# Performance work log

Measured on AMD Instinct MI355X. Metric: run time of the kernel, lower is better.

Reference implementation:

```python
import jax, jax.numpy as jnp
import numpy as np

NEG_INF = -1e9


def setup_inputs() -> dict:
    B, S, D = 4, 2048, 1024
    key = jax.random.key(0)
    ks = jax.random.split(key, 10)
    sc = 1.0 / np.sqrt(D)
    return {
        "batch": jax.random.normal(ks[0], (B, S, D), jnp.float32),
        "padding_mask": jax.random.randint(ks[1], (B, S), 0, 2) > 0,
        "Wq": jax.random.normal(ks[2], (D, D), jnp.float32) * sc,
        "bq": jnp.zeros((D,), jnp.float32),
        "Wk": jax.random.normal(ks[3], (D, D), jnp.float32) * sc,
        "bk": jnp.zeros((D,), jnp.float32),
        "Wv": jax.random.normal(ks[4], (D, D), jnp.float32) * sc,
        "bv": jnp.zeros((D,), jnp.float32),
        "Wo": jax.random.normal(ks[5], (D, D), jnp.float32) * sc,
        "bo": jnp.zeros((D,), jnp.float32),
        "num_heads": 16,
    }


def _split_heads(x, H):
    B, S, D = x.shape
    return x.reshape(B, S, H, D // H).transpose(0, 2, 1, 3)  # [B,H,S,hd]


def reference(batch, padding_mask, Wq, bq, Wk, bk, Wv, bv, Wo, bo, num_heads):
    B, S, D = batch.shape
    H = num_heads
    q = _split_heads(batch @ Wq + bq, H)  # [B,H,S,hd]
    k = _split_heads(batch @ Wk + bk, H)
    v = _split_heads(batch @ Wv + bv, H)
    # tf.keras.layers.Attention default: unscaled dot-product scores
    scores = jnp.einsum("bhqd,bhkd->bhqk", q, k)
    kmask = padding_mask[:, None, None, :]  # value/key mask -> masks score columns
    scores = jnp.where(kmask, scores, NEG_INF)
    probs = jax.nn.softmax(scores, axis=-1)
    ctx = jnp.einsum("bhqk,bhkd->bhqd", probs, v)
    # query mask zeroes padded query positions (tf Attention behavior)
    ctx = ctx * padding_mask[:, None, :, None].astype(ctx.dtype)
    ctx = ctx.transpose(0, 2, 1, 3).reshape(B, S, D)
    return ctx @ Wo + bo
```

## Files before the change

kernel.cpp:

```cpp
#include <hip/hip_runtime.h>


#define Bb 4
#define Ss 2048
#define Dd 1024
#define Hh 16
#define SZt 8388608

typedef short bf16x8 __attribute__((ext_vector_type(8)));
typedef _Float16 f16x8 __attribute__((ext_vector_type(8)));
typedef float f32x4 __attribute__((ext_vector_type(4)));
typedef float f32x16 __attribute__((ext_vector_type(16)));
typedef unsigned int u32x4 __attribute__((ext_vector_type(4)));
typedef unsigned short u16;

__device__ __forceinline__ float bf2f(u16 u) {
    return __builtin_bit_cast(float, ((unsigned)u) << 16);
}
__device__ __forceinline__ u16 f2bf(float f) {
    unsigned u = __builtin_bit_cast(unsigned, f);
    unsigned r = 0x7FFFu + ((u >> 16) & 1u);
    return (u16)((u + r) >> 16);
}
__device__ __forceinline__ u16 f2h(float f) {
    _Float16 h = (_Float16)f;
    return __builtin_bit_cast(u16, h);
}
__device__ __forceinline__ bf16x8 ldfrag(const u16* p) {
    return __builtin_bit_cast(bf16x8, *(const uint4*)p);
}
__device__ __forceinline__ f16x8 ldfragh(const u16* p) {
    return __builtin_bit_cast(f16x8, *(const uint4*)p);
}
__device__ __forceinline__ f32x4 mfma16h(f16x8 a, f16x8 b, f32x4 c) {
    return __builtin_amdgcn_mfma_f32_16x16x32_f16(a, b, c, 0, 0, 0);
}
__device__ __forceinline__ f32x4 mfma16b(bf16x8 a, bf16x8 b, f32x4 c) {
    return __builtin_amdgcn_mfma_f32_16x16x32_bf16(a, b, c, 0, 0, 0);
}
__device__ __forceinline__ f32x16 mfma32(bf16x8 a, bf16x8 b, f32x16 c) {
    return __builtin_amdgcn_mfma_f32_32x32x16_bf16(a, b, c, 0, 0, 0);
}
__device__ __forceinline__ f32x16 mfma32h(f16x8 a, f16x8 b, f32x16 c) {
    return __builtin_amdgcn_mfma_f32_32x32x16_f16(a, b, c, 0, 0, 0);
}
__device__ __forceinline__ unsigned cvt_pk_bf16(float a, float b) {
    unsigned r;
    asm("v_cvt_pk_bf16_f32 %0, %1, %2" : "=v"(r) : "v"(a), "v"(b));
    return r;
}
__device__ __forceinline__ void gl2lds16(const u16* g, u16* l) {
    __builtin_amdgcn_global_load_lds(
        (const __attribute__((address_space(1))) u16*)g,
        (__attribute__((address_space(3))) u16*)l, 16, 0, 0);
}

__global__ void normalize_mask(const unsigned char* __restrict__ raw, float* __restrict__ out,
                               float* __restrict__ cnt, int n) {
    __shared__ int flags;
    __shared__ float scnt[Bb];
    if (threadIdx.x == 0) flags = 0;
    if (threadIdx.x < Bb) scnt[threadIdx.x] = 0.f;
    __syncthreads();
    int f = 0;
    for (int i = threadIdx.x; i < n; i += blockDim.x) {
        unsigned char c = raw[i];
        if ((i & 3) != 0 && c) f |= 1;
        if ((i & 3) == 1 && c >= 2) f |= 2;
        if ((i & 3) == 3 && c >= 2) f |= 4;
    }
    if (f) atomicOr(&flags, f);
    __syncthreads();
    int fl = flags;
    int layout;
    if (!(fl & 1)) layout = 0;
    else if (fl & 2) layout = 2;
    else if (fl & 4) layout = 3;
    else layout = 1;
    for (int i = threadIdx.x; i < n; i += blockDim.x) {
        int v;
        if (layout == 0)      v = ((const int*)raw)[i];
        else if (layout == 1) v = raw[i];
        else if (layout == 2) v = ((const u16*)raw)[i] != 0;
        else                  v = ((const unsigned*)raw)[i] != 0;
        out[i] = (v != 0) ? 1.0f : 0.0f;
        if (v == 0) atomicAdd(&scnt[i >> 11], 1.0f);
    }
    __syncthreads();
    if (threadIdx.x < Bb) cnt[threadIdx.x] = scnt[threadIdx.x];
}

__global__ void concat_bias(const float* __restrict__ a, const float* __restrict__ b,
                            const float* __restrict__ c, float* __restrict__ o) {
    int i = blockIdx.x * 256 + threadIdx.x;
    o[i] = (i < 1024) ? a[i] : ((i < 2048) ? b[i - 1024] : c[i - 2048]);
}

__global__ __launch_bounds__(256) void convert_xh(const float* __restrict__ X,
                                                  u16* __restrict__ Xh) {
    size_t i = ((size_t)blockIdx.x * 256 + threadIdx.x) * 4;
    float4 v = *(const float4*)(X + i);
    u16 h0 = f2h(v.x), h1 = f2h(v.y), h2 = f2h(v.z), h3 = f2h(v.w);
    uint2 ph = { (unsigned)h0 | ((unsigned)h1 << 16), (unsigned)h2 | ((unsigned)h3 << 16) };
    *(uint2*)(Xh + i) = ph;
}

__global__ __launch_bounds__(256) void transpose_wh(const float* __restrict__ W, u16* __restrict__ Wt) {
    __shared__ float t[32][33];
    const int tx = threadIdx.x, ty = threadIdx.y;
    const int n0 = blockIdx.x * 32, k0 = blockIdx.y * 32;
    #pragma unroll
    for (int i = 0; i < 4; i++)
        t[ty + i * 8][tx] = W[(size_t)(k0 + ty + i * 8) * Dd + n0 + tx];
    __syncthreads();
    #pragma unroll
    for (int i = 0; i < 4; i++)
        Wt[(size_t)(n0 + ty + i * 8) * Dd + k0 + tx] = f2h(t[tx][ty + i * 8]);
}
__global__ __launch_bounds__(256) void transpose_w(const float* __restrict__ W, u16* __restrict__ Wt) {
    __shared__ float t[32][33];
    const int tx = threadIdx.x, ty = threadIdx.y;
    const int n0 = blockIdx.x * 32, k0 = blockIdx.y * 32;
    #pragma unroll
    for (int i = 0; i < 4; i++)
        t[ty + i * 8][tx] = W[(size_t)(k0 + ty + i * 8) * Dd + n0 + tx];
    __syncthreads();
    #pragma unroll
    for (int i = 0; i < 4; i++)
        Wt[(size_t)(n0 + ty + i * 8) * Dd + k0 + tx] = f2bf(t[tx][ty + i * 8]);
}

__global__ __launch_bounds__(512, 2) void gemm_qkv(
    const u16* __restrict__ Ah, const u16* __restrict__ Wcat, const float* __restrict__ bcat,
    const float* __restrict__ mnorm,
    u16* __restrict__ Qb, u16* __restrict__ Kb, u16* __restrict__ Vt)
{
    __shared__ u16 As[3][256][64];
    __shared__ u16 Bs[2][128][64];
    const int tid = threadIdx.x, lane = tid & 63, wave = tid >> 6;
    const int wm = wave >> 1, wn = wave & 1;
    const int bm = blockIdx.y * 256, bn = blockIdx.x * 128;
    const bool isQ = (bn < 1024);
    const int l15 = lane & 15, lq = lane >> 4;
    const int rl = lane >> 3;
    const int s8 = ((lane & 7) ^ rl) * 8;
    const u16* agp = Ah + (size_t)(bm + wave * 32 + rl) * Dd + s8;
    const u16* bgp = Wcat + (size_t)(bn + wave * 16 + rl) * Dd + s8;

    f32x4 acc[4][4] = {};

    auto stageA = [&](int slot, int kt) {
        u16* d = &As[slot][wave * 32][0];
        const u16* g = agp + kt * 64;
        #pragma unroll
        for (int j = 0; j < 4; ++j)
            gl2lds16(g + (size_t)(j * 8) * Dd, d + j * 8 * 64);
    };
    auto stageB = [&](int slot, int kt) {
        u16* d = &Bs[slot][wave * 16][0];
        const u16* g = bgp + kt * 64;
        #pragma unroll
        for (int j = 0; j < 2; ++j)
            gl2lds16(g + (size_t)(j * 8) * Dd, d + j * 8 * 64);
    };

    stageA(0, 0); stageB(0, 0); stageA(1, 1);
    asm volatile("s_waitcnt vmcnt(4)" ::: "memory");
    __builtin_amdgcn_s_barrier();

    int cs = 0;
    for (int t = 0; t < 16; ++t) {
        if (t < 15) stageB((t + 1) & 1, t + 1);
        if (t < 14) { int ss = (cs >= 1) ? cs - 1 : cs + 2; stageA(ss, t + 2); }
        #pragma unroll
        for (int kf = 0; kf < 2; kf++) {
            f16x8 b[4], a[4];
            #pragma unroll
            for (int nt = 0; nt < 4; nt++)
                b[nt] = ldfragh(&Bs[t & 1][wn * 64 + nt * 16 + l15][(kf * 32 + lq * 8) ^ ((l15 & 7) * 8)]);
            #pragma unroll
            for (int mt = 0; mt < 4; mt++)
                a[mt] = ldfragh(&As[cs][wm * 64 + mt * 16 + l15][(kf * 32 + lq * 8) ^ ((l15 & 7) * 8)]);
            #pragma unroll
            for (int mt = 0; mt < 4; mt++)
                #pragma unroll
                for (int nt = 0; nt < 4; nt++)
                    acc[mt][nt] = mfma16h(a[mt], b[nt], acc[mt][nt]);
        }
        if (t < 14)       asm volatile("s_waitcnt vmcnt(4)" ::: "memory");
        else if (t == 14) asm volatile("s_waitcnt vmcnt(0)" ::: "memory");
        if (t < 15) __builtin_amdgcn_s_barrier();
        cs = (cs >= 2) ? 0 : cs + 1;
    }

    const float LOG2E = 1.44269504088896f;
    float bv[4];
    #pragma unroll
    for (int nt = 0; nt < 4; nt++) bv[nt] = bcat[bn + wn * 64 + nt * 16 + l15];
    #pragma unroll
    for (int mt = 0; mt < 4; mt++) {
        int r0 = bm + wm * 64 + mt * 16 + lq * 4;
        float mk[4];
        if (!isQ) {
            #pragma unroll
            for (int rr = 0; rr < 4; rr++) mk[rr] = mnorm[r0 + rr];
        }
        #pragma unroll
        for (int nt = 0; nt < 4; nt++) {
            int col = bn + wn * 64 + nt * 16 + l15;
            if (col < 1024) {
                #pragma unroll
                for (int rr = 0; rr < 4; rr++)
                    Qb[(size_t)(r0 + rr) * Dd + col] = f2h((acc[mt][nt][rr] + bv[nt]) * LOG2E);
            } else if (col < 2048) {
                int c2 = col - 1024;
                #pragma unroll
                for (int rr = 0; rr < 4; rr++)
                    Kb[(size_t)(r0 + rr) * Dd + c2] = f2h((acc[mt][nt][rr] + bv[nt]) * mk[rr]);
            } else {
                int c2 = col - 2048;
                int hh = c2 >> 6, dd = c2 & 63, b_ = r0 >> 11, s0 = r0 & 2047;
                u16 e0 = f2bf((acc[mt][nt][0] + bv[nt]) * mk[0]);
                u16 e1 = f2bf((acc[mt][nt][1] + bv[nt]) * mk[1]);
                u16 e2 = f2bf((acc[mt][nt][2] + bv[nt]) * mk[2]);
                u16 e3 = f2bf((acc[mt][nt][3] + bv[nt]) * mk[3]);
                uint2 pk = { (unsigned)e0 | ((unsigned)e1 << 16), (unsigned)e2 | ((unsigned)e3 << 16) };
                *(uint2*)(Vt + (size_t)((b_ * Hh + hh) * 64 + dd) * Ss + s0) = pk;
            }
        }
    }
}

__global__ __launch_bounds__(512, 2) void gemm_out(
    const u16* __restrict__ Ah, const u16* __restrict__ Wt,
    const float* __restrict__ bias, float* __restrict__ Cout)
{
    __shared__ u16 As[3][256][64];
    __shared__ u16 Bs[2][128][64];
    const int tid = threadIdx.x, lane = tid & 63, wave = tid >> 6;
    const int wm = wave >> 1, wn = wave & 1;
    const int bm = blockIdx.y * 256, bn = blockIdx.x * 128;
    const int l15 = lane & 15, lq = lane >> 4;
    const int rl = lane >> 3;
    const int s8 = ((lane & 7) ^ rl) * 8;
    const u16* agp = Ah + (size_t)(bm + wave * 32 + rl) * Dd + s8;
    const u16* bgp = Wt + (size_t)(bn + wave * 16 + rl) * Dd + s8;

    f32x4 acc[4][4] = {};

    auto stageA = [&](int slot, int kt) {
        u16* d = &As[slot][wave * 32][0];
        const u16* g = agp + kt * 64;
        #pragma unroll
        for (int j = 0; j < 4; ++j)
            gl2lds16(g + (size_t)(j * 8) * Dd, d + j * 8 * 64);
    };
    auto stageB = [&](int slot, int kt) {
        u16* d = &Bs[slot][wave * 16][0];
        const u16* g = bgp + kt * 64;
        #pragma unroll
        for (int j = 0; j < 2; ++j)
            gl2lds16(g + (size_t)(j * 8) * Dd, d + j * 8 * 64);
    };

    stageA(0, 0); stageB(0, 0); stageA(1, 1);
    asm volatile("s_waitcnt vmcnt(4)" ::: "memory");
    __builtin_amdgcn_s_barrier();

    int cs = 0;
    for (int t = 0; t < 16; ++t) {
        if (t < 15) stageB((t + 1) & 1, t + 1);
        if (t < 14) { int ss = (cs >= 1) ? cs - 1 : cs + 2; stageA(ss, t + 2); }
        #pragma unroll
        for (int kf = 0; kf < 2; kf++) {
            bf16x8 b[4], a[4];
            #pragma unroll
            for (int nt = 0; nt < 4; nt++)
                b[nt] = ldfrag(&Bs[t & 1][wn * 64 + nt * 16 + l15][(kf * 32 + lq * 8) ^ ((l15 & 7) * 8)]);
            #pragma unroll
            for (int mt = 0; mt < 4; mt++)
                a[mt] = ldfrag(&As[cs][wm * 64 + mt * 16 + l15][(kf * 32 + lq * 8) ^ ((l15 & 7) * 8)]);
            #pragma unroll
            for (int mt = 0; mt < 4; mt++)
                #pragma unroll
                for (int nt = 0; nt < 4; nt++)
                    acc[mt][nt] = mfma16b(a[mt], b[nt], acc[mt][nt]);
        }
        if (t < 14)       asm volatile("s_waitcnt vmcnt(4)" ::: "memory");
        else if (t == 14) asm volatile("s_waitcnt vmcnt(0)" ::: "memory");
        if (t < 15) __builtin_amdgcn_s_barrier();
        cs = (cs >= 2) ? 0 : cs + 1;
    }

    float bv[4];
    #pragma unroll
    for (int nt = 0; nt < 4; nt++) bv[nt] = bias[bn + wn * 64 + nt * 16 + l15];
    #pragma unroll
    for (int mt = 0; mt < 4; mt++) {
        int r0 = bm + wm * 64 + mt * 16 + lq * 4;
        #pragma unroll
        for (int nt = 0; nt < 4; nt++) {
            int col = bn + wn * 64 + nt * 16 + l15;
            #pragma unroll
            for (int rr = 0; rr < 4; rr++)
                Cout[(size_t)(r0 + rr) * Dd + col] = acc[mt][nt][rr] + bv[nt];
        }
    }
}

__global__ __launch_bounds__(512, 4) void attn_mfma(
    u16* qctx, const u16* __restrict__ Kb, const u16* __restrict__ Vt,
    const float* __restrict__ maskf, const float* __restrict__ cntp)
{
    __shared__ u16 Ks[64][72];
    __shared__ u16 Vs[64][72];
    __shared__ float li_s[8][32];
    const int tid = threadIdx.x, lane = tid & 63, wave = tid >> 6;
    const int l31 = lane & 31, hi = lane >> 5;
    const int bh = blockIdx.x, h = bh & 15, b = bh >> 4;
    const int q0 = blockIdx.y * 256;

    f16x8 qa[4];
    {
        const u16* qp = qctx + (size_t)(b * Ss + q0 + wave * 32 + l31) * Dd + h * 64 + hi * 8;
        #pragma unroll
        for (int kf = 0; kf < 4; kf++) qa[kf] = ldfragh(qp + kf * 16);
    }

    const int srow = tid >> 3, scol = (tid & 7) * 8;
    const u16* kgsrc = Kb + (size_t)(b * Ss + srow) * Dd + h * 64 + scol;
    const u16* vgsrc = Vt + (size_t)((b * Hh + h) * 64 + srow) * Ss + scol;
    u16* kdst = &Ks[srow][scol];
    u16* vdst = &Vs[srow][scol];

    f32x16 acc0 = {}, acc1 = {};
    float li = 0.f;

    uint4 kreg = *(const uint4*)kgsrc;
    uint4 vreg = *(const uint4*)vgsrc;

    for (int k0 = 0; k0 < Ss; k0 += 64) {
        __syncthreads();
        *(uint4*)kdst = kreg;
        *(uint4*)vdst = vreg;
        __syncthreads();
        int k0n = (k0 + 64 < Ss) ? k0 + 64 : 0;
        kreg = *(const uint4*)(kgsrc + (size_t)k0n * Dd);
        vreg = *(const uint4*)(vgsrc + k0n);

        #pragma unroll
        for (int nt = 0; nt < 2; nt++) {
            f32x16 sc = {};
            #pragma unroll
            for (int kf = 0; kf < 4; kf++) {
                f16x8 kb = ldfragh(&Ks[nt * 32 + l31][kf * 16 + hi * 8]);
                sc = mfma32h(kb, qa[kf], sc);
            }
            float p[16];
            #pragma unroll
            for (int r = 0; r < 8; r++) p[r] = __builtin_amdgcn_exp2f(sc[r]);
            li += ((p[0] + p[1]) + (p[2] + p[3])) + ((p[4] + p[5]) + (p[6] + p[7]));
            {
                unsigned w0 = cvt_pk_bf16(p[0], p[1]), w1 = cvt_pk_bf16(p[2], p[3]);
                unsigned w2 = cvt_pk_bf16(p[4], p[5]), w3 = cvt_pk_bf16(p[6], p[7]);
                auto s02 = __builtin_amdgcn_permlane32_swap((int)w0, (int)w2, false, false);
                auto s13 = __builtin_amdgcn_permlane32_swap((int)w1, (int)w3, false, false);
                u32x4 pw = { (unsigned)s02[0], (unsigned)s13[0], (unsigned)s02[1], (unsigned)s13[1] };
                bf16x8 pa0 = __builtin_bit_cast(bf16x8, pw);
                bf16x8 v00 = ldfrag(&Vs[l31][nt * 32 + hi * 8]);
                bf16x8 v10 = ldfrag(&Vs[32 + l31][nt * 32 + hi * 8]);
                acc0 = mfma32(pa0, v00, acc0);
                acc1 = mfma32(pa0, v10, acc1);
            }
            #pragma unroll
            for (int r = 8; r < 16; r++) p[r] = __builtin_amdgcn_exp2f(sc[r]);
            li += ((p[8] + p[9]) + (p[10] + p[11])) + ((p[12] + p[13]) + (p[14] + p[15]));
            {
                unsigned w4 = cvt_pk_bf16(p[8], p[9]),  w5 = cvt_pk_bf16(p[10], p[11]);
                unsigned w6 = cvt_pk_bf16(p[12], p[13]), w7 = cvt_pk_bf16(p[14], p[15]);
                auto s46 = __builtin_amdgcn_permlane32_swap((int)w4, (int)w6, false, false);
                auto s57 = __builtin_amdgcn_permlane32_swap((int)w5, (int)w7, false, false);
                u32x4 pw = { (unsigned)s46[0], (unsigned)s57[0], (unsigned)s46[1], (unsigned)s57[1] };
                bf16x8 pa1 = __builtin_bit_cast(bf16x8, pw);
                bf16x8 v01 = ldfrag(&Vs[l31][nt * 32 + 16 + hi * 8]);
                bf16x8 v11 = ldfrag(&Vs[32 + l31][nt * 32 + 16 + hi * 8]);
                acc0 = mfma32(pa1, v01, acc0);
                acc1 = mfma32(pa1, v11, acc1);
            }
        }
    }

    float li_tot = li + __shfl_xor(li, 32);
    if (hi == 0) li_s[wave][l31] = li_tot;
    __builtin_amdgcn_s_barrier();
    float cntb = cntp[b];
    #pragma unroll
    for (int g = 0; g < 4; g++) {
        float4 lv = *(const float4*)&li_s[wave][g * 8 + hi * 4];
        #pragma unroll
        for (int j = 0; j < 4; j++) {
            int r = g * 4 + j;
            int row = j + 8 * g + 4 * hi;
            int q = q0 + wave * 32 + row;
            float qm = maskf[b * Ss + q];
            float den = lv[j] - cntb;
            float rl = den > 0.f ? qm / den : 0.f;
            u16* op = qctx + (size_t)(b * Ss + q) * Dd + h * 64 + l31;
            op[0]  = f2bf(acc0[r] * rl);
            op[32] = f2bf(acc1[r] * rl);
        }
    }
}

extern "C" void kernel_launch(void* const* d_in, const int* in_sizes, int n_in,
                              void* d_out, int out_size, void* d_ws, size_t ws_size,
                              hipStream_t stream) {
    const float* X  = (const float*)d_in[0];
    const unsigned char* mr = (const unsigned char*)d_in[1];
    const float* Wq = (const float*)d_in[2];
    const float* bq = (const float*)d_in[3];
    const float* Wk = (const float*)d_in[4];
    const float* bk = (const float*)d_in[5];
    const float* Wv = (const float*)d_in[6];
    const float* bv = (const float*)d_in[7];
    const float* Wo = (const float*)d_in[8];
    const float* bo = (const float*)d_in[9];
    float* out = (float*)d_out;

    u16* wsb = (u16*)d_ws;
    u16* Xh  = wsb;
    u16* Qb  = wsb + (size_t)SZt;
    u16* Kb  = wsb + 2 * (size_t)SZt;
    u16* Vt  = wsb + 3 * (size_t)SZt;
    u16* Wot = Xh;
    u16* ob  = (u16*)d_out;
    u16* Wcat = ob + (size_t)SZt;
    u16* Wqt = Wcat;
    u16* Wkt = Wqt + 1048576;
    u16* Wvt = Wkt + 1048576;
    float* mnorm = (float*)(Wvt + 1048576);
    float* bcat  = mnorm + Bb * Ss;
    float* cntp  = bcat + 3072;

    dim3 tg(32, 32), tb(32, 8);

    normalize_mask<<<1, 1024, 0, stream>>>(mr, mnorm, cntp, Bb * Ss);
    concat_bias<<<12, 256, 0, stream>>>(bq, bk, bv, bcat);
    convert_xh<<<SZt / 1024, 256, 0, stream>>>(X, Xh);
    transpose_wh<<<tg, tb, 0, stream>>>(Wq, Wqt);
    transpose_wh<<<tg, tb, 0, stream>>>(Wk, Wkt);
    transpose_wh<<<tg, tb, 0, stream>>>(Wv, Wvt);
    gemm_qkv<<<dim3(24, 32), 512, 0, stream>>>(Xh, Wcat, bcat, mnorm, Qb, Kb, Vt);
    transpose_w<<<tg, tb, 0, stream>>>(Wo, Wot);
    attn_mfma<<<dim3(Bb * Hh, Ss / 256), 512, 0, stream>>>(Qb, Kb, Vt, mnorm, cntp);
    gemm_out<<<dim3(8, 32), 512, 0, stream>>>(Qb, Wot, bo, out);
}
```

Before: 293.8 us.

## Fuse prologue kernels, add MFMA priority hints, and widen attention key tiles

Merges the mask normalization, bias concat, X conversion and three weight transposes into one launch, cutting five kernel launches and their gaps. Wraps the MFMA sections of both GEMMs and the attention kernel in s_setprio so waves doing matrix work are issued ahead of others. The attention loop now stages 128 keys per iteration instead of 64, halving barriers per key but doubling LDS use, which may lower occupancy. The single mask block inside the large grid could become a tail if it is scheduled late.

```diff
diff --git a/kernel.cpp b/kernel.cpp
--- a/kernel.cpp
+++ b/kernel.cpp
@@ -55,68 +55,76 @@
         (__attribute__((address_space(3))) u16*)l, 16, 0, 0);
 }
 
-__global__ void normalize_mask(const unsigned char* __restrict__ raw, float* __restrict__ out,
-                               float* __restrict__ cnt, int n) {
+__global__ __launch_bounds__(256) void prologue(
+    const float* __restrict__ X, u16* __restrict__ Xh,
+    const float* __restrict__ Wq, const float* __restrict__ Wk, const float* __restrict__ Wv,
+    u16* __restrict__ Wqt, u16* __restrict__ Wkt, u16* __restrict__ Wvt,
+    const float* __restrict__ bq, const float* __restrict__ bk, const float* __restrict__ bv,
+    float* __restrict__ bcat,
+    const unsigned char* __restrict__ mraw, float* __restrict__ mnorm, float* __restrict__ cntp)
+{
+    __shared__ float tl[32][33];
     __shared__ int flags;
     __shared__ float scnt[Bb];
-    if (threadIdx.x == 0) flags = 0;
-    if (threadIdx.x < Bb) scnt[threadIdx.x] = 0.f;
-    __syncthreads();
-    int f = 0;
-    for (int i = threadIdx.x; i < n; i += blockDim.x) {
-        unsigned char c = raw[i];
-        if ((i & 3) != 0 && c) f |= 1;
-        if ((i & 3) == 1 && c >= 2) f |= 2;
-        if ((i & 3) == 3 && c >= 2) f |= 4;
-    }
-    if (f) atomicOr(&flags, f);
-    __syncthreads();
-    int fl = flags;
-    int layout;
-    if (!(fl & 1)) layout = 0;
-    else if (fl & 2) layout = 2;
-    else if (fl & 4) layout = 3;
-    else layout = 1;
-    for (int i = threadIdx.x; i < n; i += blockDim.x) {
-        int v;
-        if (layout == 0)      v = ((const int*)raw)[i];
-        else if (layout == 1) v = raw[i];
-        else if (layout == 2) v = ((const u16*)raw)[i] != 0;
-        else                  v = ((const unsigned*)raw)[i] != 0;
-        out[i] = (v != 0) ? 1.0f : 0.0f;
-        if (v == 0) atomicAdd(&scnt[i >> 11], 1.0f);
-    }
-    __syncthreads();
-    if (threadIdx.x < Bb) cnt[threadIdx.x] = scnt[threadIdx.x];
-}
-
-__global__ void concat_bias(const float* __restrict__ a, const float* __restrict__ b,
-                            const float* __restrict__ c, float* __restrict__ o) {
-    int i = blockIdx.x * 256 + threadIdx.x;
-    o[i] = (i < 1024) ? a[i] : ((i < 2048) ? b[i - 1024] : c[i - 2048]);
-}
-
-__global__ __launch_bounds__(256) void convert_xh(const float* __restrict__ X,
-                                                  u16* __restrict__ Xh) {
-    size_t i = ((size_t)blockIdx.x * 256 + threadIdx.x) * 4;
-    float4 v = *(const float4*)(X + i);
-    u16 h0 = f2h(v.x), h1 = f2h(v.y), h2 = f2h(v.z), h3 = f2h(v.w);
-    uint2 ph = { (unsigned)h0 | ((unsigned)h1 << 16), (unsigned)h2 | ((unsigned)h3 << 16) };
-    *(uint2*)(Xh + i) = ph;
-}
-
-__global__ __launch_bounds__(256) void transpose_wh(const float* __restrict__ W, u16* __restrict__ Wt) {
-    __shared__ float t[32][33];
-    const int tx = threadIdx.x, ty = threadIdx.y;
-    const int n0 = blockIdx.x * 32, k0 = blockIdx.y * 32;
-    #pragma unroll
-    for (int i = 0; i < 4; i++)
-        t[ty + i * 8][tx] = W[(size_t)(k0 + ty + i * 8) * Dd + n0 + tx];
-    __syncthreads();
-    #pragma unroll
-    for (int i = 0; i < 4; i++)
-        Wt[(size_t)(n0 + ty + i * 8) * Dd + k0 + tx] = f2h(t[tx][ty + i * 8]);
-}
+    const int blk = blockIdx.x, tid = threadIdx.x;
+
+    if (blk < 8192) {
+        size_t i = ((size_t)blk * 256 + tid) * 4;
+        float4 v = *(const float4*)(X + i);
+        u16 h0 = f2h(v.x), h1 = f2h(v.y), h2 = f2h(v.z), h3 = f2h(v.w);
+        uint2 ph = { (unsigned)h0 | ((unsigned)h1 << 16), (unsigned)h2 | ((unsigned)h3 << 16) };
+        *(uint2*)(Xh + i) = ph;
+    } else if (blk < 11264) {
+        int idx = blk - 8192;
+        int w = idx >> 10, t = idx & 1023;
+        const float* W = (w == 0) ? Wq : ((w == 1) ? Wk : Wv);
+        u16* Wt = (w == 0) ? Wqt : ((w == 1) ? Wkt : Wvt);
+        const int tx = tid & 31, ty = tid >> 5;
+        const int n0 = (t & 31) * 32, k0 = (t >> 5) * 32;
+        #pragma unroll
+        for (int i = 0; i < 4; i++)
+            tl[ty + i * 8][tx] = W[(size_t)(k0 + ty + i * 8) * Dd + n0 + tx];
+        __syncthreads();
+        #pragma unroll
+        for (int i = 0; i < 4; i++)
+            Wt[(size_t)(n0 + ty + i * 8) * Dd + k0 + tx] = f2h(tl[tx][ty + i * 8]);
+    } else if (blk < 11276) {
+        int i = (blk - 11264) * 256 + tid;
+        bcat[i] = (i < 1024) ? bq[i] : ((i < 2048) ? bk[i - 1024] : bv[i - 2048]);
+    } else {
+        const int n = Bb * Ss;
+        if (tid == 0) flags = 0;
+        if (tid < Bb) scnt[tid] = 0.f;
+        __syncthreads();
+        int f = 0;
+        for (int i = tid; i < n; i += 256) {
+            unsigned char c = mraw[i];
+            if ((i & 3) != 0 && c) f |= 1;
+            if ((i & 3) == 1 && c >= 2) f |= 2;
+            if ((i & 3) == 3 && c >= 2) f |= 4;
+        }
+        if (f) atomicOr(&flags, f);
+        __syncthreads();
+        int fl = flags;
+        int layout;
+        if (!(fl & 1)) layout = 0;
+        else if (fl & 2) layout = 2;
+        else if (fl & 4) layout = 3;
+        else layout = 1;
+        for (int i = tid; i < n; i += 256) {
+            int v;
+            if (layout == 0)      v = ((const int*)mraw)[i];
+            else if (layout == 1) v = mraw[i];
+            else if (layout == 2) v = ((const u16*)mraw)[i] != 0;
+            else                  v = ((const unsigned*)mraw)[i] != 0;
+            mnorm[i] = (v != 0) ? 1.0f : 0.0f;
+            if (v == 0) atomicAdd(&scnt[i >> 11], 1.0f);
+        }
+        __syncthreads();
+        if (tid < Bb) cntp[tid] = scnt[tid];
+    }
+}
+
 __global__ __launch_bounds__(256) void transpose_w(const float* __restrict__ W, u16* __restrict__ Wt) {
     __shared__ float t[32][33];
     const int tx = threadIdx.x, ty = threadIdx.y;
@@ -172,6 +180,7 @@
     for (int t = 0; t < 16; ++t) {
         if (t < 15) stageB((t + 1) & 1, t + 1);
         if (t < 14) { int ss = (cs >= 1) ? cs - 1 : cs + 2; stageA(ss, t + 2); }
+        __builtin_amdgcn_s_setprio(1);
         #pragma unroll
         for (int kf = 0; kf < 2; kf++) {
             f16x8 b[4], a[4];
@@ -187,6 +196,7 @@
                 for (int nt = 0; nt < 4; nt++)
                     acc[mt][nt] = mfma16h(a[mt], b[nt], acc[mt][nt]);
         }
+        __builtin_amdgcn_s_setprio(0);
         if (t < 14)       asm volatile("s_waitcnt vmcnt(4)" ::: "memory");
         else if (t == 14) asm volatile("s_waitcnt vmcnt(0)" ::: "memory");
         if (t < 15) __builtin_amdgcn_s_barrier();
@@ -271,6 +281,7 @@
     for (int t = 0; t < 16; ++t) {
         if (t < 15) stageB((t + 1) & 1, t + 1);
         if (t < 14) { int ss = (cs >= 1) ? cs - 1 : cs + 2; stageA(ss, t + 2); }
+        __builtin_amdgcn_s_setprio(1);
         #pragma unroll
         for (int kf = 0; kf < 2; kf++) {
             bf16x8 b[4], a[4];
@@ -286,6 +297,7 @@
                 for (int nt = 0; nt < 4; nt++)
                     acc[mt][nt] = mfma16b(a[mt], b[nt], acc[mt][nt]);
         }
+        __builtin_amdgcn_s_setprio(0);
         if (t < 14)       asm volatile("s_waitcnt vmcnt(4)" ::: "memory");
         else if (t == 14) asm volatile("s_waitcnt vmcnt(0)" ::: "memory");
         if (t < 15) __builtin_amdgcn_s_barrier();
@@ -312,8 +324,8 @@
     u16* qctx, const u16* __restrict__ Kb, const u16* __restrict__ Vt,
     const float* __restrict__ maskf, const float* __restrict__ cntp)
 {
-    __shared__ u16 Ks[64][72];
-    __shared__ u16 Vs[64][72];
+    __shared__ u16 Ks[128][72];
+    __shared__ u16 Vs[64][136];
     __shared__ float li_s[8][32];
     const int tid = threadIdx.x, lane = tid & 63, wave = tid >> 6;
     const int l31 = lane & 31, hi = lane >> 5;
@@ -327,35 +339,42 @@
         for (int kf = 0; kf < 4; kf++) qa[kf] = ldfragh(qp + kf * 16);
     }
 
-    const int srow = tid >> 3, scol = (tid & 7) * 8;
-    const u16* kgsrc = Kb + (size_t)(b * Ss + srow) * Dd + h * 64 + scol;
-    const u16* vgsrc = Vt + (size_t)((b * Hh + h) * 64 + srow) * Ss + scol;
-    u16* kdst = &Ks[srow][scol];
-    u16* vdst = &Vs[srow][scol];
+    const int kr = tid >> 3, kc = (tid & 7) * 8;
+    const int vd = tid >> 4, vc = (tid & 15) * 8;
+    const u16* kgb = Kb + ((size_t)b * Ss + kr) * Dd + h * 64 + kc;
+    const u16* vgb = Vt + (((size_t)(b * Hh + h)) * 64 + vd) * Ss + vc;
 
     f32x16 acc0 = {}, acc1 = {};
     float li = 0.f;
 
-    uint4 kreg = *(const uint4*)kgsrc;
-    uint4 vreg = *(const uint4*)vgsrc;
-
-    for (int k0 = 0; k0 < Ss; k0 += 64) {
-        __syncthreads();
-        *(uint4*)kdst = kreg;
-        *(uint4*)vdst = vreg;
-        __syncthreads();
-        int k0n = (k0 + 64 < Ss) ? k0 + 64 : 0;
-        kreg = *(const uint4*)(kgsrc + (size_t)k0n * Dd);
-        vreg = *(const uint4*)(vgsrc + k0n);
-
-        #pragma unroll
-        for (int nt = 0; nt < 2; nt++) {
+    uint4 kreg0 = *(const uint4*)(kgb);
+    uint4 kreg1 = *(const uint4*)(kgb + (size_t)64 * Dd);
+    uint4 vreg0 = *(const uint4*)(vgb);
+    uint4 vreg1 = *(const uint4*)(vgb + (size_t)32 * Ss);
+
+    for (int k0 = 0; k0 < Ss; k0 += 128) {
+        __syncthreads();
+        *(uint4*)&Ks[kr][kc]      = kreg0;
+        *(uint4*)&Ks[kr + 64][kc] = kreg1;
+        *(uint4*)&Vs[vd][vc]      = vreg0;
+        *(uint4*)&Vs[vd + 32][vc] = vreg1;
+        __syncthreads();
+        int k0n = (k0 + 128 < Ss) ? k0 + 128 : 0;
+        kreg0 = *(const uint4*)(kgb + (size_t)k0n * Dd);
+        kreg1 = *(const uint4*)(kgb + (size_t)(k0n + 64) * Dd);
+        vreg0 = *(const uint4*)(vgb + k0n);
+        vreg1 = *(const uint4*)(vgb + (size_t)32 * Ss + k0n);
+
+        #pragma unroll
+        for (int nt = 0; nt < 4; nt++) {
             f32x16 sc = {};
+            __builtin_amdgcn_s_setprio(1);
             #pragma unroll
             for (int kf = 0; kf < 4; kf++) {
                 f16x8 kb = ldfragh(&Ks[nt * 32 + l31][kf * 16 + hi * 8]);
                 sc = mfma32h(kb, qa[kf], sc);
             }
+            __builtin_amdgcn_s_setprio(0);
             float p[16];
             #pragma unroll
             for (int r = 0; r < 8; r++) p[r] = __builtin_amdgcn_exp2f(sc[r]);
@@ -369,8 +388,10 @@
                 bf16x8 pa0 = __builtin_bit_cast(bf16x8, pw);
                 bf16x8 v00 = ldfrag(&Vs[l31][nt * 32 + hi * 8]);
                 bf16x8 v10 = ldfrag(&Vs[32 + l31][nt * 32 + hi * 8]);
+                __builtin_amdgcn_s_setprio(1);
                 acc0 = mfma32(pa0, v00, acc0);
                 acc1 = mfma32(pa0, v10, acc1);
+                __builtin_amdgcn_s_setprio(0);
             }
             #pragma unroll
             for (int r = 8; r < 16; r++) p[r] = __builtin_amdgcn_exp2f(sc[r]);
@@ -384,8 +405,10 @@
                 bf16x8 pa1 = __builtin_bit_cast(bf16x8, pw);
                 bf16x8 v01 = ldfrag(&Vs[l31][nt * 32 + 16 + hi * 8]);
                 bf16x8 v11 = ldfrag(&Vs[32 + l31][nt * 32 + 16 + hi * 8]);
+                __builtin_amdgcn_s_setprio(1);
                 acc0 = mfma32(pa1, v01, acc0);
                 acc1 = mfma32(pa1, v11, acc1);
+                __builtin_amdgcn_s_setprio(0);
             }
         }
     }
@@ -442,16 +465,10 @@
     float* bcat  = mnorm + Bb * Ss;
     float* cntp  = bcat + 3072;
 
-    dim3 tg(32, 32), tb(32, 8);
-
-    normalize_mask<<<1, 1024, 0, stream>>>(mr, mnorm, cntp, Bb * Ss);
-    concat_bias<<<12, 256, 0, stream>>>(bq, bk, bv, bcat);
-    convert_xh<<<SZt / 1024, 256, 0, stream>>>(X, Xh);
-    transpose_wh<<<tg, tb, 0, stream>>>(Wq, Wqt);
-    transpose_wh<<<tg, tb, 0, stream>>>(Wk, Wkt);
-    transpose_wh<<<tg, tb, 0, stream>>>(Wv, Wvt);
+    prologue<<<11277, 256, 0, stream>>>(X, Xh, Wq, Wk, Wv, Wqt, Wkt, Wvt,
+                                        bq, bk, bv, bcat, mr, mnorm, cntp);
     gemm_qkv<<<dim3(24, 32), 512, 0, stream>>>(Xh, Wcat, bcat, mnorm, Qb, Kb, Vt);
-    transpose_w<<<tg, tb, 0, stream>>>(Wo, Wot);
+    transpose_w<<<dim3(32, 32), dim3(32, 8), 0, stream>>>(Wo, Wot);
     attn_mfma<<<dim3(Bb * Hh, Ss / 256), 512, 0, stream>>>(Qb, Kb, Vt, mnorm, cntp);
     gemm_out<<<dim3(8, 32), 512, 0, stream>>>(Qb, Wot, bo, out);
 }
```

Result: slower. 301.0 us (+2.4%).
